# Kernel tuning notes

Hardware: AMD Instinct MI355X
Metric: run time of the kernel (lower is better)

## Reference

```python
import jax, jax.numpy as jnp
import numpy as np

BBOX_NORMALIZE_STDS = jnp.array([0.1, 0.1, 0.2, 0.2], dtype=jnp.float32)
BBOX_NORMALIZE_MEANS = jnp.array([0.0, 0.0, 0.0, 0.0], dtype=jnp.float32)
THRESH = 0.05


def setup_inputs() -> dict:
    key = jax.random.key(0)
    k1, k2, k3, k4 = jax.random.split(key, 4)
    N, C = 1_000_000, 7
    H, W = 600.0, 1000.0
    u = jax.random.uniform(k1, (N, 4), dtype=jnp.float32)
    x1 = u[:, 0] * (W - 60.0)
    y1 = u[:, 1] * (H - 60.0)
    x2 = x1 + u[:, 2] * 50.0 + 8.0
    y2 = y1 + u[:, 3] * 50.0 + 8.0
    boxes = jnp.stack([x1, y1, x2, y2], axis=1)  # [N,4] valid rois in image coords
    box_deltas = jax.random.normal(k2, (N, 4 * C), dtype=jnp.float32) * 0.5
    scores = jax.nn.softmax(jax.random.normal(k3, (N, C), dtype=jnp.float32) * 2.0, axis=1)
    im_info = jnp.array([H, W, 1.0], dtype=jnp.float32)
    return {"boxes": boxes, "box_deltas": box_deltas, "scores": scores, "im_info": im_info}


def _decode_clip(boxes, box_deltas, im_info):
    # de-normalize deltas (applied per 4-vector as in the torch code: view(-1,4)*stds+means)
    N = boxes.shape[0]
    C = box_deltas.shape[1] // 4
    deltas = (box_deltas.reshape(-1, 4) * BBOX_NORMALIZE_STDS + BBOX_NORMALIZE_MEANS).reshape(N, C, 4)
    # bbox_transform_inv
    widths = boxes[:, 2] - boxes[:, 0] + 1.0
    heights = boxes[:, 3] - boxes[:, 1] + 1.0
    ctr_x = boxes[:, 0] + 0.5 * widths
    ctr_y = boxes[:, 1] + 0.5 * heights
    dx, dy, dw, dh = deltas[..., 0], deltas[..., 1], deltas[..., 2], deltas[..., 3]
    pred_ctr_x = dx * widths[:, None] + ctr_x[:, None]
    pred_ctr_y = dy * heights[:, None] + ctr_y[:, None]
    pred_w = jnp.exp(dw) * widths[:, None]
    pred_h = jnp.exp(dh) * heights[:, None]
    x1 = pred_ctr_x - 0.5 * pred_w
    y1 = pred_ctr_y - 0.5 * pred_h
    x2 = pred_ctr_x + 0.5 * pred_w
    y2 = pred_ctr_y + 0.5 * pred_h
    # clip_boxes to image (im_info = [H, W, scale])
    x1 = jnp.clip(x1, 0.0, im_info[1] - 1.0)
    x2 = jnp.clip(x2, 0.0, im_info[1] - 1.0)
    y1 = jnp.clip(y1, 0.0, im_info[0] - 1.0)
    y2 = jnp.clip(y2, 0.0, im_info[0] - 1.0)
    return jnp.stack([x1, y1, x2, y2], axis=-1)  # [N, C, 4]


def _pick_region(pred, scores, cls_ids):
    # per-class threshold + best-score selection (vectorized replacement of the
    # torch nonzero/sort loop: only the top-scoring det per class is ever kept)
    s = scores[:, cls_ids]                      # [N, k]
    masked = jnp.where(s > THRESH, s, -1.0)     # below-threshold -> never selected
    idx = jnp.argmax(masked, axis=0)            # [k] best proposal per class
    b = pred[idx, cls_ids]                      # [k, 4] class-specific boxes
    sc = masked[idx, jnp.arange(cls_ids.shape[0])]
    dets = jnp.concatenate([b, sc[:, None]], axis=1)  # [k, 5]
    best = jnp.argmax(dets[:, -1])
    return dets[best]                           # [5]


def reference(boxes, box_deltas, scores, im_info):
    pred = _decode_clip(boxes, box_deltas, im_info)        # [N, C, 4]
    pred_boxes = pred.reshape(pred.shape[0], -1)           # [N, 4*C]
    region_g = _pick_region(pred, scores, jnp.array([1, 2, 3]))
    region_l = _pick_region(pred, scores, jnp.array([4, 5, 6]))
    return pred_boxes, region_g, region_l
```

## Files before the change

### kernel.cpp

```cpp
#include <hip/hip_runtime.h>
#include <hip/hip_bf16.h>


#define THRESH_F 0.05f
#define NCLS 7
#define BLOCKS 2048
#define TPB 256

__device__ __forceinline__ unsigned map_float(unsigned bits) {
    return (bits & 0x80000000u) ? ~bits : (bits | 0x80000000u);
}

__global__ __launch_bounds__(TPB) void decode_pick_kernel(
    const float4* __restrict__ boxes,
    const float4* __restrict__ deltas,
    const float*  __restrict__ scores,
    const float*  __restrict__ im_info,
    float4*       __restrict__ pred,
    unsigned long long* __restrict__ blockbest,
    int NP)
{
    __shared__ unsigned long long sbest[6];
    const int tid = threadIdx.x;
    if (tid < 6) sbest[tid] = 0ULL;
    __syncthreads();

    const float maxX = im_info[1] - 1.0f;
    const float maxY = im_info[0] - 1.0f;

    const int stride = gridDim.x * blockDim.x;
    for (int p = blockIdx.x * blockDim.x + tid; p < NP; p += stride) {
        const unsigned up = (unsigned)p;
        const unsigned i  = up / 7u;
        const unsigned c  = up - i * 7u;

        const float4 d = deltas[p];
        const float4 b = boxes[i];

        const float w  = b.z - b.x + 1.0f;
        const float h  = b.w - b.y + 1.0f;
        const float cx = b.x + 0.5f * w;
        const float cy = b.y + 0.5f * h;

        const float pcx = (d.x * 0.1f) * w + cx;
        const float pcy = (d.y * 0.1f) * h + cy;
        const float pw  = __expf(d.z * 0.2f) * w * 0.5f;
        const float ph  = __expf(d.w * 0.2f) * h * 0.5f;

        float4 o;
        o.x = fminf(fmaxf(pcx - pw, 0.0f), maxX);
        o.y = fminf(fmaxf(pcy - ph, 0.0f), maxY);
        o.z = fminf(fmaxf(pcx + pw, 0.0f), maxX);
        o.w = fminf(fmaxf(pcy + ph, 0.0f), maxY);
        pred[p] = o;

        if (c != 0u) {
            const float s = scores[p];
            const float m = (s > THRESH_F) ? s : -1.0f;
            const unsigned mapped = map_float(__float_as_uint(m));
            const unsigned long long key =
                ((unsigned long long)mapped << 32) |
                (unsigned long long)(0xFFFFFFFFu - i);
            const int slot = (int)c - 1;
            const unsigned curhi = ((volatile unsigned*)sbest)[slot * 2 + 1];
            if (mapped >= curhi)
                atomicMax(&sbest[slot], key);
        }
    }
    __syncthreads();
    if (tid < 6)
        blockbest[(size_t)blockIdx.x * 6 + tid] = sbest[tid];
}

__global__ __launch_bounds__(TPB) void finalize_kernel(
    const unsigned long long* __restrict__ blockbest,
    int nblocks,
    const float* __restrict__ pred,
    float*       __restrict__ regions)
{
    __shared__ unsigned long long red[TPB];
    __shared__ unsigned long long fin[6];
    const int tid = threadIdx.x;

    for (int slot = 0; slot < 6; ++slot) {
        unsigned long long k = 0ULL;
        for (int j = tid; j < nblocks; j += TPB) {
            unsigned long long v = blockbest[(size_t)j * 6 + slot];
            k = (v > k) ? v : k;
        }
        red[tid] = k;
        __syncthreads();
        for (int off = TPB / 2; off > 0; off >>= 1) {
            if (tid < off) {
                unsigned long long v = red[tid + off];
                if (v > red[tid]) red[tid] = v;
            }
            __syncthreads();
        }
        if (tid == 0) fin[slot] = red[0];
        __syncthreads();
    }

    if (tid == 0) {
        for (int g = 0; g < 2; ++g) {
            float scores_[3];
            unsigned idx_[3];
            float bestScore = -1e30f;
            int bestJ = 0;
            for (int j = 0; j < 3; ++j) {
                const unsigned long long key = fin[g * 3 + j];
                const unsigned hi = (unsigned)(key >> 32);
                const unsigned bits = (hi & 0x80000000u) ? (hi & 0x7FFFFFFFu) : ~hi;
                const float sc = __uint_as_float(bits);
                const unsigned idx = 0xFFFFFFFFu - (unsigned)(key & 0xFFFFFFFFu);
                scores_[j] = sc;
                idx_[j] = idx;
                if (sc > bestScore) { bestScore = sc; bestJ = j; }
            }
            const int c = g * 3 + bestJ + 1;
            const unsigned i = idx_[bestJ];
            const float* pb = pred + (size_t)i * 28 + (size_t)c * 4;
            float* r = regions + g * 5;
            r[0] = pb[0];
            r[1] = pb[1];
            r[2] = pb[2];
            r[3] = pb[3];
            r[4] = scores_[bestJ];
        }
    }
}

extern "C" void kernel_launch(void* const* d_in, const int* in_sizes, int n_in,
                              void* d_out, int out_size, void* d_ws, size_t ws_size,
                              hipStream_t stream) {
    const float* boxes   = (const float*)d_in[0];
    const float* deltas  = (const float*)d_in[1];
    const float* scores  = (const float*)d_in[2];
    const float* im_info = (const float*)d_in[3];

    const int N  = in_sizes[0] / 4;
    const int NP = N * NCLS;

    float* out = (float*)d_out;
    float* regions = out + (size_t)N * 4 * NCLS;

    unsigned long long* blockbest = (unsigned long long*)d_ws;

    decode_pick_kernel<<<BLOCKS, TPB, 0, stream>>>(
        (const float4*)boxes, (const float4*)deltas, scores, im_info,
        (float4*)out, blockbest, NP);

    finalize_kernel<<<1, TPB, 0, stream>>>(blockbest, BLOCKS, out, regions);
}
```

Baseline: 243.5 us.

## Fuse finalize into decode kernel via global atomics and last-block reduction

Replaces the grid-stride decode kernel and separate single-block finalize kernel with one kernel. Each block handles a fixed 4 items per thread with all loads issued up front, and writes outputs with nontemporal stores. Per-class bests are merged with global 64-bit atomicMax, and the last block to finish (tracked by an atomic counter) recomputes the two chosen boxes directly from the inputs. This removes a kernel launch and the blockbest round trip, at the cost of a memset per call, many more blocks, and global atomic contention.

```diff
diff --git a/kernel.cpp b/kernel.cpp
--- a/kernel.cpp
+++ b/kernel.cpp
@@ -3,24 +3,50 @@
 
 
 #define THRESH_F 0.05f
-#define NCLS 7
-#define BLOCKS 2048
 #define TPB 256
+#define ITEMS 4
+
+typedef __attribute__((ext_vector_type(4))) float f4raw;
 
 __device__ __forceinline__ unsigned map_float(unsigned bits) {
     return (bits & 0x80000000u) ? ~bits : (bits | 0x80000000u);
 }
+__device__ __forceinline__ float unmap_float(unsigned m) {
+    unsigned bits = (m & 0x80000000u) ? (m & 0x7FFFFFFFu) : ~m;
+    return __uint_as_float(bits);
+}
 
-__global__ __launch_bounds__(TPB) void decode_pick_kernel(
+__device__ __forceinline__ float4 decode_one(float4 b, float4 d,
+                                             float maxX, float maxY) {
+    const float w  = b.z - b.x + 1.0f;
+    const float h  = b.w - b.y + 1.0f;
+    const float cx = b.x + 0.5f * w;
+    const float cy = b.y + 0.5f * h;
+    const float pcx = (d.x * 0.1f) * w + cx;
+    const float pcy = (d.y * 0.1f) * h + cy;
+    const float pw  = __expf(d.z * 0.2f) * w * 0.5f;
+    const float ph  = __expf(d.w * 0.2f) * h * 0.5f;
+    float4 o;
+    o.x = fminf(fmaxf(pcx - pw, 0.0f), maxX);
+    o.y = fminf(fmaxf(pcy - ph, 0.0f), maxY);
+    o.z = fminf(fmaxf(pcx + pw, 0.0f), maxX);
+    o.w = fminf(fmaxf(pcy + ph, 0.0f), maxY);
+    return o;
+}
+
+__global__ __launch_bounds__(TPB) void fused_kernel(
     const float4* __restrict__ boxes,
     const float4* __restrict__ deltas,
     const float*  __restrict__ scores,
     const float*  __restrict__ im_info,
     float4*       __restrict__ pred,
-    unsigned long long* __restrict__ blockbest,
+    unsigned long long* __restrict__ gslots,
+    unsigned*           __restrict__ counter,
+    float*              __restrict__ regions,
     int NP)
 {
     __shared__ unsigned long long sbest[6];
+    __shared__ int isLast;
     const int tid = threadIdx.x;
     if (tid < 6) sbest[tid] = 0ULL;
     __syncthreads();
@@ -28,104 +54,79 @@
     const float maxX = im_info[1] - 1.0f;
     const float maxY = im_info[0] - 1.0f;
 
-    const int stride = gridDim.x * blockDim.x;
-    for (int p = blockIdx.x * blockDim.x + tid; p < NP; p += stride) {
-        const unsigned up = (unsigned)p;
-        const unsigned i  = up / 7u;
-        const unsigned c  = up - i * 7u;
+    const int base = blockIdx.x * (TPB * ITEMS) + tid;
 
-        const float4 d = deltas[p];
-        const float4 b = boxes[i];
+    int      p[ITEMS];
+    bool     valid[ITEMS];
+    unsigned ii[ITEMS], cc[ITEMS];
+    float4   d[ITEMS], bx[ITEMS];
+    float    sc[ITEMS];
 
-        const float w  = b.z - b.x + 1.0f;
-        const float h  = b.w - b.y + 1.0f;
-        const float cx = b.x + 0.5f * w;
-        const float cy = b.y + 0.5f * h;
+    #pragma unroll
+    for (int k = 0; k < ITEMS; ++k) {
+        p[k]     = base + k * TPB;
+        valid[k] = (p[k] < NP);
+        const int pc = valid[k] ? p[k] : 0;
+        const unsigned up = (unsigned)pc;
+        ii[k] = up / 7u;
+        cc[k] = up - ii[k] * 7u;
+        d[k]  = deltas[pc];
+        bx[k] = boxes[ii[k]];
+        sc[k] = scores[pc];
+    }
 
-        const float pcx = (d.x * 0.1f) * w + cx;
-        const float pcy = (d.y * 0.1f) * h + cy;
-        const float pw  = __expf(d.z * 0.2f) * w * 0.5f;
-        const float ph  = __expf(d.w * 0.2f) * h * 0.5f;
+    #pragma unroll
+    for (int k = 0; k < ITEMS; ++k) {
+        if (!valid[k]) continue;
+        const float4 o = decode_one(bx[k], d[k], maxX, maxY);
+        f4raw r; r.x = o.x; r.y = o.y; r.z = o.z; r.w = o.w;
+        __builtin_nontemporal_store(r, (f4raw*)(pred + p[k]));
 
-        float4 o;
-        o.x = fminf(fmaxf(pcx - pw, 0.0f), maxX);
-        o.y = fminf(fmaxf(pcy - ph, 0.0f), maxY);
-        o.z = fminf(fmaxf(pcx + pw, 0.0f), maxX);
-        o.w = fminf(fmaxf(pcy + ph, 0.0f), maxY);
-        pred[p] = o;
-
-        if (c != 0u) {
-            const float s = scores[p];
-            const float m = (s > THRESH_F) ? s : -1.0f;
+        if (cc[k] != 0u) {
+            const float m = (sc[k] > THRESH_F) ? sc[k] : -1.0f;
             const unsigned mapped = map_float(__float_as_uint(m));
             const unsigned long long key =
                 ((unsigned long long)mapped << 32) |
-                (unsigned long long)(0xFFFFFFFFu - i);
-            const int slot = (int)c - 1;
+                (unsigned long long)(0xFFFFFFFFu - ii[k]);
+            const int slot = (int)cc[k] - 1;
             const unsigned curhi = ((volatile unsigned*)sbest)[slot * 2 + 1];
             if (mapped >= curhi)
                 atomicMax(&sbest[slot], key);
         }
     }
     __syncthreads();
-    if (tid < 6)
-        blockbest[(size_t)blockIdx.x * 6 + tid] = sbest[tid];
-}
 
-__global__ __launch_bounds__(TPB) void finalize_kernel(
-    const unsigned long long* __restrict__ blockbest,
-    int nblocks,
-    const float* __restrict__ pred,
-    float*       __restrict__ regions)
-{
-    __shared__ unsigned long long red[TPB];
-    __shared__ unsigned long long fin[6];
-    const int tid = threadIdx.x;
-
-    for (int slot = 0; slot < 6; ++slot) {
-        unsigned long long k = 0ULL;
-        for (int j = tid; j < nblocks; j += TPB) {
-            unsigned long long v = blockbest[(size_t)j * 6 + slot];
-            k = (v > k) ? v : k;
-        }
-        red[tid] = k;
-        __syncthreads();
-        for (int off = TPB / 2; off > 0; off >>= 1) {
-            if (tid < off) {
-                unsigned long long v = red[tid + off];
-                if (v > red[tid]) red[tid] = v;
-            }
-            __syncthreads();
-        }
-        if (tid == 0) fin[slot] = red[0];
-        __syncthreads();
+    if (tid < 6) {
+        if (sbest[tid] != 0ULL)
+            atomicMax(&gslots[tid], sbest[tid]);
+        __threadfence();
     }
+    __syncthreads();
 
     if (tid == 0) {
+        const unsigned prev = atomicAdd(counter, 1u);
+        isLast = (prev == gridDim.x - 1u);
+    }
+    __syncthreads();
+
+    if (isLast && tid == 0) {
+        __threadfence();
         for (int g = 0; g < 2; ++g) {
-            float scores_[3];
-            unsigned idx_[3];
-            float bestScore = -1e30f;
+            float bestSc = -1e30f;
             int bestJ = 0;
+            unsigned bestIdx = 0;
             for (int j = 0; j < 3; ++j) {
-                const unsigned long long key = fin[g * 3 + j];
-                const unsigned hi = (unsigned)(key >> 32);
-                const unsigned bits = (hi & 0x80000000u) ? (hi & 0x7FFFFFFFu) : ~hi;
-                const float sc = __uint_as_float(bits);
+                const unsigned long long key = atomicMax(&gslots[g * 3 + j], 0ULL);
+                const float s = unmap_float((unsigned)(key >> 32));
                 const unsigned idx = 0xFFFFFFFFu - (unsigned)(key & 0xFFFFFFFFu);
-                scores_[j] = sc;
-                idx_[j] = idx;
-                if (sc > bestScore) { bestScore = sc; bestJ = j; }
+                if (s > bestSc) { bestSc = s; bestJ = j; bestIdx = idx; }
             }
             const int c = g * 3 + bestJ + 1;
-            const unsigned i = idx_[bestJ];
-            const float* pb = pred + (size_t)i * 28 + (size_t)c * 4;
+            const float4 b  = boxes[bestIdx];
+            const float4 dd = deltas[bestIdx * 7u + (unsigned)c];
+            const float4 o  = decode_one(b, dd, maxX, maxY);
             float* r = regions + g * 5;
-            r[0] = pb[0];
-            r[1] = pb[1];
-            r[2] = pb[2];
-            r[3] = pb[3];
-            r[4] = scores_[bestJ];
+            r[0] = o.x; r[1] = o.y; r[2] = o.z; r[3] = o.w; r[4] = bestSc;
         }
     }
 }
@@ -139,16 +140,18 @@
     const float* im_info = (const float*)d_in[3];
 
     const int N  = in_sizes[0] / 4;
-    const int NP = N * NCLS;
+    const int NP = N * 7;
 
     float* out = (float*)d_out;
-    float* regions = out + (size_t)N * 4 * NCLS;
+    float* regions = out + (size_t)N * 28;
 
-    unsigned long long* blockbest = (unsigned long long*)d_ws;
+    unsigned long long* gslots = (unsigned long long*)d_ws;
+    unsigned* counter = (unsigned*)((char*)d_ws + 48);
 
-    decode_pick_kernel<<<BLOCKS, TPB, 0, stream>>>(
+    hipMemsetAsync(d_ws, 0, 64, stream);
+
+    const int nblk = (NP + TPB * ITEMS - 1) / (TPB * ITEMS);
+    fused_kernel<<<nblk, TPB, 0, stream>>>(
         (const float4*)boxes, (const float4*)deltas, scores, im_info,
-        (float4*)out, blockbest, NP);
-
-    finalize_kernel<<<1, TPB, 0, stream>>>(blockbest, BLOCKS, out, regions);
+        (float4*)out, gslots, counter, regions, NP);
 }
```

Measured after the change: 541.3 us. 2.22x slower.

## Process one row per thread and reduce the per-class best with wave shuffles

Applied to the files above, without the earlier changes.

The decode kernel now assigns whole proposals to threads: each thread loads its box once, reads all 7 delta float4s and 6 scores, and decodes the 7 classes in an unrolled loop. Per-class best keys are kept in registers, reduced across each wavefront with xor shuffles, and combined with one shared atomic per wave per slot. This replaces per-element shared-memory atomics and the divide-by-7 index math. The trade-off is that each load and store instruction is strided by 112 bytes rather than coalesced, and register pressure goes up. The grid is now sized from N instead of a fixed block count.

```diff
diff --git a/kernel.cpp b/kernel.cpp
--- a/kernel.cpp
+++ b/kernel.cpp
@@ -3,9 +3,11 @@
 
 
 #define THRESH_F 0.05f
-#define NCLS 7
-#define BLOCKS 2048
 #define TPB 256
+#define RPT 2
+#define ROWS_PER_BLOCK (TPB * RPT)
+
+typedef unsigned long long ull;
 
 __device__ __forceinline__ unsigned map_float(unsigned bits) {
     return (bits & 0x80000000u) ? ~bits : (bits | 0x80000000u);
@@ -17,55 +19,77 @@
     const float*  __restrict__ scores,
     const float*  __restrict__ im_info,
     float4*       __restrict__ pred,
-    unsigned long long* __restrict__ blockbest,
-    int NP)
+    ull*          __restrict__ blockbest,
+    int N)
 {
-    __shared__ unsigned long long sbest[6];
     const int tid = threadIdx.x;
-    if (tid < 6) sbest[tid] = 0ULL;
-    __syncthreads();
-
     const float maxX = im_info[1] - 1.0f;
     const float maxY = im_info[0] - 1.0f;
 
-    const int stride = gridDim.x * blockDim.x;
-    for (int p = blockIdx.x * blockDim.x + tid; p < NP; p += stride) {
-        const unsigned up = (unsigned)p;
-        const unsigned i  = up / 7u;
-        const unsigned c  = up - i * 7u;
+    ull best[6];
+    #pragma unroll
+    for (int s = 0; s < 6; ++s) best[s] = 0ULL;
 
-        const float4 d = deltas[p];
-        const float4 b = boxes[i];
+    for (int r = 0; r < RPT; ++r) {
+        const int row = blockIdx.x * ROWS_PER_BLOCK + r * TPB + tid;
+        if (row >= N) continue;
+
+        const float4 b = boxes[row];
+        const float4* __restrict__ drow = deltas + (size_t)row * 7;
+        float4 d[7];
+        #pragma unroll
+        for (int c = 0; c < 7; ++c) d[c] = drow[c];
+        const float* __restrict__ srow = scores + (size_t)row * 7;
+        float s[6];
+        #pragma unroll
+        for (int c = 0; c < 6; ++c) s[c] = srow[c + 1];
 
         const float w  = b.z - b.x + 1.0f;
         const float h  = b.w - b.y + 1.0f;
         const float cx = b.x + 0.5f * w;
         const float cy = b.y + 0.5f * h;
 
-        const float pcx = (d.x * 0.1f) * w + cx;
-        const float pcy = (d.y * 0.1f) * h + cy;
-        const float pw  = __expf(d.z * 0.2f) * w * 0.5f;
-        const float ph  = __expf(d.w * 0.2f) * h * 0.5f;
+        float4* __restrict__ prow = pred + (size_t)row * 7;
+        const unsigned negrow = 0xFFFFFFFFu - (unsigned)row;
 
-        float4 o;
-        o.x = fminf(fmaxf(pcx - pw, 0.0f), maxX);
-        o.y = fminf(fmaxf(pcy - ph, 0.0f), maxY);
-        o.z = fminf(fmaxf(pcx + pw, 0.0f), maxX);
-        o.w = fminf(fmaxf(pcy + ph, 0.0f), maxY);
-        pred[p] = o;
+        #pragma unroll
+        for (int c = 0; c < 7; ++c) {
+            const float pcx = (d[c].x * 0.1f) * w + cx;
+            const float pcy = (d[c].y * 0.1f) * h + cy;
+            const float pw  = __expf(d[c].z * 0.2f) * w * 0.5f;
+            const float ph  = __expf(d[c].w * 0.2f) * h * 0.5f;
+            float4 o;
+            o.x = fminf(fmaxf(pcx - pw, 0.0f), maxX);
+            o.y = fminf(fmaxf(pcy - ph, 0.0f), maxY);
+            o.z = fminf(fmaxf(pcx + pw, 0.0f), maxX);
+            o.w = fminf(fmaxf(pcy + ph, 0.0f), maxY);
+            prow[c] = o;
 
-        if (c != 0u) {
-            const float s = scores[p];
-            const float m = (s > THRESH_F) ? s : -1.0f;
-            const unsigned mapped = map_float(__float_as_uint(m));
-            const unsigned long long key =
-                ((unsigned long long)mapped << 32) |
-                (unsigned long long)(0xFFFFFFFFu - i);
-            const int slot = (int)c - 1;
-            const unsigned curhi = ((volatile unsigned*)sbest)[slot * 2 + 1];
-            if (mapped >= curhi)
-                atomicMax(&sbest[slot], key);
+            if (c >= 1) {
+                const float m = (s[c - 1] > THRESH_F) ? s[c - 1] : -1.0f;
+                const ull key = ((ull)map_float(__float_as_uint(m)) << 32) |
+                                (ull)negrow;
+                if (key > best[c - 1]) best[c - 1] = key;
+            }
         }
+    }
+
+    #pragma unroll
+    for (int slot = 0; slot < 6; ++slot) {
+        #pragma unroll
+        for (int off = 32; off > 0; off >>= 1) {
+            const ull v = __shfl_xor(best[slot], off, 64);
+            if (v > best[slot]) best[slot] = v;
+        }
+    }
+
+    __shared__ ull sbest[6];
+    if (tid < 6) sbest[tid] = 0ULL;
+    __syncthreads();
+    if ((tid & 63) == 0) {
+        #pragma unroll
+        for (int slot = 0; slot < 6; ++slot)
+            if (best[slot] != 0ULL) atomicMax(&sbest[slot], best[slot]);
     }
     __syncthreads();
     if (tid < 6)
@@ -73,26 +97,26 @@
 }
 
 __global__ __launch_bounds__(TPB) void finalize_kernel(
-    const unsigned long long* __restrict__ blockbest,
+    const ull* __restrict__ blockbest,
     int nblocks,
     const float* __restrict__ pred,
     float*       __restrict__ regions)
 {
-    __shared__ unsigned long long red[TPB];
-    __shared__ unsigned long long fin[6];
+    __shared__ ull red[TPB];
+    __shared__ ull fin[6];
     const int tid = threadIdx.x;
 
     for (int slot = 0; slot < 6; ++slot) {
-        unsigned long long k = 0ULL;
+        ull k = 0ULL;
         for (int j = tid; j < nblocks; j += TPB) {
-            unsigned long long v = blockbest[(size_t)j * 6 + slot];
-            k = (v > k) ? v : k;
+            const ull v = blockbest[(size_t)j * 6 + slot];
+            if (v > k) k = v;
         }
         red[tid] = k;
         __syncthreads();
         for (int off = TPB / 2; off > 0; off >>= 1) {
             if (tid < off) {
-                unsigned long long v = red[tid + off];
+                const ull v = red[tid + off];
                 if (v > red[tid]) red[tid] = v;
             }
             __syncthreads();
@@ -108,14 +132,12 @@
             float bestScore = -1e30f;
             int bestJ = 0;
             for (int j = 0; j < 3; ++j) {
-                const unsigned long long key = fin[g * 3 + j];
+                const ull key = fin[g * 3 + j];
                 const unsigned hi = (unsigned)(key >> 32);
                 const unsigned bits = (hi & 0x80000000u) ? (hi & 0x7FFFFFFFu) : ~hi;
-                const float sc = __uint_as_float(bits);
-                const unsigned idx = 0xFFFFFFFFu - (unsigned)(key & 0xFFFFFFFFu);
-                scores_[j] = sc;
-                idx_[j] = idx;
-                if (sc > bestScore) { bestScore = sc; bestJ = j; }
+                scores_[j] = __uint_as_float(bits);
+                idx_[j] = 0xFFFFFFFFu - (unsigned)(key & 0xFFFFFFFFu);
+                if (scores_[j] > bestScore) { bestScore = scores_[j]; bestJ = j; }
             }
             const int c = g * 3 + bestJ + 1;
             const unsigned i = idx_[bestJ];
@@ -138,17 +160,17 @@
     const float* scores  = (const float*)d_in[2];
     const float* im_info = (const float*)d_in[3];
 
-    const int N  = in_sizes[0] / 4;
-    const int NP = N * NCLS;
+    const int N = in_sizes[0] / 4;
 
     float* out = (float*)d_out;
-    float* regions = out + (size_t)N * 4 * NCLS;
+    float* regions = out + (size_t)N * 28;
 
-    unsigned long long* blockbest = (unsigned long long*)d_ws;
+    ull* blockbest = (ull*)d_ws;
 
-    decode_pick_kernel<<<BLOCKS, TPB, 0, stream>>>(
+    const int nblk = (N + ROWS_PER_BLOCK - 1) / ROWS_PER_BLOCK;
+    decode_pick_kernel<<<nblk, TPB, 0, stream>>>(
         (const float4*)boxes, (const float4*)deltas, scores, im_info,
-        (float4*)out, blockbest, NP);
+        (float4*)out, blockbest, N);
 
-    finalize_kernel<<<1, TPB, 0, stream>>>(blockbest, BLOCKS, out, regions);
+    finalize_kernel<<<1, TPB, 0, stream>>>(blockbest, nblk, out, regions);
 }
```

New measurement: 272.8 us. 1.12x slower.
